# Kernel tuning notes

Measured on AMD Instinct MI355X. Metric: run time of the kernel, lower is better.

## Reference

```python
import jax, jax.numpy as jnp
import numpy as np

BLOCKSIZE = 64
# Fixed NF4 codebook (bitsandbytes normal-float 4-bit quantiles)
NF4_CODE = jnp.array([
    -1.0, -0.6961928009986877, -0.5250730514526367, -0.39491748809814453,
    -0.28444138169288635, -0.18477343022823334, -0.09105003625154495, 0.0,
    0.07958029955625534, 0.16093020141124725, 0.24611230194568634,
    0.33791524171829224, 0.44070982933044434, 0.5626170039176941,
    0.7229568362236023, 1.0], dtype=jnp.float32)


def setup_inputs() -> dict:
    key = jax.random.key(0)
    k1, k2, k3, k4 = jax.random.split(key, 4)
    B, IN, OUT = 32, 4096, 14336
    x = jax.random.normal(k1, (B, IN), dtype=jnp.float32)
    codes = jax.random.randint(k2, (OUT, IN), 0, 16, dtype=jnp.int32)
    absmax = jax.random.uniform(k3, (OUT * IN // BLOCKSIZE,), dtype=jnp.float32)
    bias = jax.random.normal(k4, (OUT,), dtype=jnp.float32)
    return {"x": x, "codes": codes, "absmax": absmax, "bias": bias}


def reference(x, codes, absmax, bias):
    out_f, in_f = codes.shape
    # Dequantize: codebook lookup then per-block (64) absmax scaling
    w = NF4_CODE[codes].reshape(-1, BLOCKSIZE) * absmax[:, None]  # [nblocks, 64]
    w = w.reshape(out_f, in_f)
    # y = x @ W^T + bias  (matmul_4bit semantics)
    return jnp.einsum('bi,oi->bo', x, w) + bias
```

## Files before the change

kernel.cpp:

```cpp
#include <hip/hip_runtime.h>
#include <stddef.h>
#include <stdint.h>

#define B_   32
#define IN_  4096
#define OUT_ 14336

typedef short v8s __attribute__((ext_vector_type(8)));
typedef float v4f __attribute__((ext_vector_type(4)));

__device__ __constant__ float c_nf4[16] = {
    -1.0f, -0.6961928009986877f, -0.5250730514526367f, -0.39491748809814453f,
    -0.28444138169288635f, -0.18477343022823334f, -0.09105003625154495f, 0.0f,
    0.07958029955625534f, 0.16093020141124725f, 0.24611230194568634f,
    0.33791524171829224f, 0.44070982933044434f, 0.5626170039176941f,
    0.7229568362236023f, 1.0f};

__device__ __forceinline__ unsigned f2bf_u(float f) {
    union { float f; unsigned u; } v; v.f = f;
    return (v.u + 0x7FFFu + ((v.u >> 16) & 1u)) >> 16;
}
__device__ __forceinline__ unsigned pack2(float lo, float hi) {
    return f2bf_u(lo) | (f2bf_u(hi) << 16);
}

__global__ __launch_bounds__(256) void prep(const float* __restrict__ x,
                                            unsigned* __restrict__ xB) {
    int t  = blockIdx.x * 256 + threadIdx.x;
    int kt = t >> 7;
    int bt = (t >> 6) & 1;
    int l  = t & 63;
    int b  = bt * 16 + (l & 15);
    int k0 = kt * 32 + (l >> 4) * 8;
    const float* xr = x + (size_t)b * IN_ + k0;
    float4 a = *(const float4*)xr;
    float4 c = *(const float4*)(xr + 4);
    uint4 w;
    w.x = pack2(a.x, a.y);
    w.y = pack2(a.z, a.w);
    w.z = pack2(c.x, c.y);
    w.w = pack2(c.z, c.w);
    *(uint4*)(xB + (size_t)t * 4) = w;
}

__global__ __launch_bounds__(256) void nf4_mfma(
    const int* __restrict__ codes, const float* __restrict__ absmax,
    const unsigned* __restrict__ xB, const float* __restrict__ bias,
    float* __restrict__ out) {
    __shared__ float lut[16];
    if (threadIdx.x < 16) lut[threadIdx.x] = c_nf4[threadIdx.x];
    __syncthreads();

    const int w  = threadIdx.x >> 6;
    const int l  = threadIdx.x & 63;
    const int o0 = blockIdx.x * 64 + w * 16;
    const int m  = l & 15;
    const int q  = l >> 4;

    const int*   crow  = codes + (size_t)(o0 + m) * IN_ + q * 8;
    const float* amrow = absmax + (size_t)(o0 + m) * 64;
    const uint4* xbp   = (const uint4*)xB + l;

    v4f acc0 = {0.f, 0.f, 0.f, 0.f};
    v4f acc1 = {0.f, 0.f, 0.f, 0.f};

#pragma unroll 4
    for (int kt = 0; kt < 128; ++kt) {
        int4 c0 = *(const int4*)(crow + (size_t)kt * 32);
        int4 c1 = *(const int4*)(crow + (size_t)kt * 32 + 4);
        uint4 b0 = xbp[(size_t)kt * 128];
        uint4 b1 = xbp[(size_t)kt * 128 + 64];
        float am = amrow[kt >> 1];

        union { uint4 u; v8s v; } a, f0, f1;
        a.u.x = pack2(lut[c0.x] * am, lut[c0.y] * am);
        a.u.y = pack2(lut[c0.z] * am, lut[c0.w] * am);
        a.u.z = pack2(lut[c1.x] * am, lut[c1.y] * am);
        a.u.w = pack2(lut[c1.z] * am, lut[c1.w] * am);
        f0.u = b0;
        f1.u = b1;
        acc0 = __builtin_amdgcn_mfma_f32_16x16x32_bf16(a.v, f0.v, acc0, 0, 0, 0);
        acc1 = __builtin_amdgcn_mfma_f32_16x16x32_bf16(a.v, f1.v, acc1, 0, 0, 0);
    }

    const int bc = l & 15;
    const int ob = o0 + q * 4;
#pragma unroll
    for (int r = 0; r < 4; ++r) {
        float bv = bias[ob + r];
        out[(size_t)bc * OUT_ + ob + r]        = acc0[r] + bv;
        out[(size_t)(bc + 16) * OUT_ + ob + r] = acc1[r] + bv;
    }
}

extern "C" void kernel_launch(void* const* d_in, const int* in_sizes, int n_in,
                              void* d_out, int out_size, void* d_ws, size_t ws_size,
                              hipStream_t stream) {
    const float* x      = (const float*)d_in[0];
    const int*   codes  = (const int*)d_in[1];
    const float* absmax = (const float*)d_in[2];
    const float* bias   = (const float*)d_in[3];
    float* out = (float*)d_out;
    unsigned* xB = (unsigned*)d_ws;

    prep<<<dim3(64), 256, 0, stream>>>(x, xB);
    nf4_mfma<<<dim3(OUT_ / 64), 256, 0, stream>>>(codes, absmax, xB, bias, out);
}
```

Baseline: 323.9 us.

## Split-K the NF4 MFMA kernel across 8 slices with partial-sum reduction

Splits the K dimension into 8 slices so the grid grows from 224 to 1792 workgroups, giving the GPU's many CUs more work to hide the memory latency of streaming the int32 codes. Partial results go to a workspace buffer and a separate reduce kernel sums them and adds the bias. If the workspace is too small, it falls back to initializing the output with bias and using atomic adds. It also sets a launch-bounds occupancy hint. The cost is extra partial-buffer traffic (8x32x14336 floats) and an additional kernel launch.

```diff
diff --git a/kernel.cpp b/kernel.cpp
--- a/kernel.cpp
+++ b/kernel.cpp
@@ -2,9 +2,13 @@
 #include <stddef.h>
 #include <stdint.h>
 
-#define B_   32
-#define IN_  4096
-#define OUT_ 14336
+#define B_     32
+#define IN_    4096
+#define OUT_   14336
+#define KSPLIT 8
+#define KRANGE (IN_ / KSPLIT)
+#define NSTEP  (KRANGE / 32)
+#define POUT   (B_ * OUT_)
 
 typedef short v8s __attribute__((ext_vector_type(8)));
 typedef float v4f __attribute__((ext_vector_type(4)));
@@ -43,29 +47,52 @@
     *(uint4*)(xB + (size_t)t * 4) = w;
 }
 
-__global__ __launch_bounds__(256) void nf4_mfma(
+__global__ __launch_bounds__(256) void init_out(const float* __restrict__ bias,
+                                                float* __restrict__ out) {
+    int i4 = (blockIdx.x * 256 + threadIdx.x) * 4;
+    int o = i4 % OUT_;
+    *(float4*)(out + i4) = *(const float4*)(bias + o);
+}
+
+__global__ __launch_bounds__(256) void reduce_out(const float* __restrict__ partial,
+                                                  const float* __restrict__ bias,
+                                                  float* __restrict__ out) {
+    int i4 = (blockIdx.x * 256 + threadIdx.x) * 4;
+    int o = i4 % OUT_;
+    float4 r = *(const float4*)(bias + o);
+#pragma unroll
+    for (int s = 0; s < KSPLIT; ++s) {
+        float4 p = *(const float4*)(partial + (size_t)s * POUT + i4);
+        r.x += p.x; r.y += p.y; r.z += p.z; r.w += p.w;
+    }
+    *(float4*)(out + i4) = r;
+}
+
+template <int ATOMIC>
+__global__ __launch_bounds__(256, 4) void nf4_mfma(
     const int* __restrict__ codes, const float* __restrict__ absmax,
-    const unsigned* __restrict__ xB, const float* __restrict__ bias,
-    float* __restrict__ out) {
+    const unsigned* __restrict__ xB, float* __restrict__ dst) {
     __shared__ float lut[16];
     if (threadIdx.x < 16) lut[threadIdx.x] = c_nf4[threadIdx.x];
     __syncthreads();
 
     const int w  = threadIdx.x >> 6;
     const int l  = threadIdx.x & 63;
-    const int o0 = blockIdx.x * 64 + w * 16;
+    const int ot = blockIdx.x >> 3;
+    const int ks = blockIdx.x & 7;
+    const int o0 = ot * 64 + w * 16;
     const int m  = l & 15;
     const int q  = l >> 4;
 
-    const int*   crow  = codes + (size_t)(o0 + m) * IN_ + q * 8;
-    const float* amrow = absmax + (size_t)(o0 + m) * 64;
-    const uint4* xbp   = (const uint4*)xB + l;
+    const int*   crow  = codes + (size_t)(o0 + m) * IN_ + ks * KRANGE + q * 8;
+    const float* amrow = absmax + (size_t)(o0 + m) * 64 + ks * (KRANGE / 64);
+    const uint4* xbp   = (const uint4*)xB + (size_t)(ks * NSTEP) * 128 + l;
 
     v4f acc0 = {0.f, 0.f, 0.f, 0.f};
     v4f acc1 = {0.f, 0.f, 0.f, 0.f};
 
 #pragma unroll 4
-    for (int kt = 0; kt < 128; ++kt) {
+    for (int kt = 0; kt < NSTEP; ++kt) {
         int4 c0 = *(const int4*)(crow + (size_t)kt * 32);
         int4 c1 = *(const int4*)(crow + (size_t)kt * 32 + 4);
         uint4 b0 = xbp[(size_t)kt * 128];
@@ -87,9 +114,13 @@
     const int ob = o0 + q * 4;
 #pragma unroll
     for (int r = 0; r < 4; ++r) {
-        float bv = bias[ob + r];
-        out[(size_t)bc * OUT_ + ob + r]        = acc0[r] + bv;
-        out[(size_t)(bc + 16) * OUT_ + ob + r] = acc1[r] + bv;
+        if (ATOMIC) {
+            atomicAdd(dst + (size_t)bc * OUT_ + ob + r, acc0[r]);
+            atomicAdd(dst + (size_t)(bc + 16) * OUT_ + ob + r, acc1[r]);
+        } else {
+            dst[((size_t)ks * B_ + bc) * OUT_ + ob + r]      = acc0[r];
+            dst[((size_t)ks * B_ + bc + 16) * OUT_ + ob + r] = acc1[r];
+        }
     }
 }
 
@@ -104,5 +135,14 @@
     unsigned* xB = (unsigned*)d_ws;
 
     prep<<<dim3(64), 256, 0, stream>>>(x, xB);
-    nf4_mfma<<<dim3(OUT_ / 64), 256, 0, stream>>>(codes, absmax, xB, bias, out);
+
+    const size_t need = 262144 + (size_t)KSPLIT * POUT * 4;
+    if (ws_size >= need) {
+        float* partial = (float*)((char*)d_ws + 262144);
+        nf4_mfma<0><<<dim3(224 * KSPLIT), 256, 0, stream>>>(codes, absmax, xB, partial);
+        reduce_out<<<dim3(POUT / 1024), 256, 0, stream>>>(partial, bias, out);
+    } else {
+        init_out<<<dim3(POUT / 1024), 256, 0, stream>>>(bias, out);
+        nf4_mfma<1><<<dim3(224 * KSPLIT), 256, 0, stream>>>(codes, absmax, xB, out);
+    }
 }
```

After: 334.5 us. 1.03x slower.
